# Performance work log

Hardware: AMD Instinct MI355X
Metric: run time of the kernel (lower is better)

Reference implementation:

```python
import jax, jax.numpy as jnp
import numpy as np

B, L, D, H = 2, 2048, 1024, 16
HD = D // H

def setup_inputs() -> dict:
    key = jax.random.key(0)
    ks = jax.random.split(key, 9)
    s = 1.0 / np.sqrt(D)
    return {
        "query": jax.random.normal(ks[0], (B, L, D), dtype=jnp.float32),
        "Wq": jax.random.uniform(ks[1], (D, D), jnp.float32, -s, s),
        "bq": jax.random.uniform(ks[2], (D,), jnp.float32, -s, s),
        "Wk": jax.random.uniform(ks[3], (D, D), jnp.float32, -s, s),
        "bk": jax.random.uniform(ks[4], (D,), jnp.float32, -s, s),
        "Wv": jax.random.uniform(ks[5], (D, D), jnp.float32, -s, s),
        "bv": jax.random.uniform(ks[6], (D,), jnp.float32, -s, s),
        "Wo": jax.random.uniform(ks[7], (D, D), jnp.float32, -s, s),
        "bo": jax.random.uniform(ks[8], (D,), jnp.float32, -s, s),
    }

def reference(query, Wq, bq, Wk, bk, Wv, bv, Wo, bo):
    # self-attention: key_value = query. Linear: x @ W.T + b (torch convention)
    scale = HD ** -0.5
    q = (query @ Wq.T + bq).reshape(B, L, H, HD).transpose(0, 2, 1, 3)  # (B,H,L,hd)
    k = (query @ Wk.T + bk).reshape(B, L, H, HD).transpose(0, 2, 1, 3)
    v = (query @ Wv.T + bv).reshape(B, L, H, HD).transpose(0, 2, 1, 3)
    logits = jnp.einsum('bhqd,bhkd->bhqk', q, k) * scale  # (B,H,Lq,Lk)
    attn = jax.nn.softmax(logits, axis=-1)
    out = jnp.einsum('bhqk,bhkd->bhqd', attn, v)
    out = out.transpose(0, 2, 1, 3).reshape(B, L, D)
    return out @ Wo.T + bo
```

## Files before the change

kernel.cpp:

```cpp
#include <hip/hip_runtime.h>

#define Bc 2
#define Lc 2048
#define Dc 1024
#define Hc 16
#define HDc 64
#define LOG2E 1.44269504088896340736f

typedef __bf16 bf16x8 __attribute__((ext_vector_type(8)));
typedef __bf16 bf16x2 __attribute__((ext_vector_type(2)));
typedef float f32x4 __attribute__((ext_vector_type(4)));
typedef unsigned short u16;
typedef unsigned int u32;
typedef unsigned long long u64;

__device__ __forceinline__ u16 f2bf(float x) {
    union { float f; u32 u; } c; c.f = x;
    u32 u = c.u + 0x7fffu + ((c.u >> 16) & 1u);
    return (u16)(u >> 16);
}

__device__ __forceinline__ u32 pkbf(float a, float b) {
#if __has_builtin(__builtin_amdgcn_cvt_pk_bf16_f32)
    union { bf16x2 v; u32 u; } c;
    c.v = __builtin_amdgcn_cvt_pk_bf16_f32(a, b);
    return c.u;
#else
    return (u32)f2bf(a) | ((u32)f2bf(b) << 16);
#endif
}

__device__ __forceinline__ void g2l16(const void* g, void* l) {
    __builtin_amdgcn_global_load_lds(
        (const __attribute__((address_space(1))) void*)g,
        (__attribute__((address_space(3))) void*)l, 16, 0, 0);
}

__global__ __launch_bounds__(256) void cast_bf16(
    const float* __restrict__ x,
    const float* __restrict__ wq, const float* __restrict__ wk,
    const float* __restrict__ wv, const float* __restrict__ wo,
    u16* __restrict__ xb, u16* __restrict__ wqb, u16* __restrict__ wkb,
    u16* __restrict__ wvb, u16* __restrict__ wob)
{
    const int i = blockIdx.x * 256 + threadIdx.x;
    const float* s; u16* d; int off;
    if (i < 1048576) { s = x; d = xb; off = i; }
    else {
        const int j = i - 1048576;
        const int sel = j >> 18;
        off = j & 262143;
        s = sel == 0 ? wq : sel == 1 ? wk : sel == 2 ? wv : wo;
        d = sel == 0 ? wqb : sel == 1 ? wkb : sel == 2 ? wvb : wob;
    }
    const float4 f = ((const float4*)s)[off];
    ushort4 o;
    o.x = f2bf(f.x); o.y = f2bf(f.y); o.z = f2bf(f.z); o.w = f2bf(f.w);
    ((ushort4*)d)[off] = o;
}

__device__ __forceinline__ void gemm128_body(
    const u16* __restrict__ A, const u16* __restrict__ Bm,
    int row0, int col0, int K,
    f32x4 (&acc)[4][4], u16* As, u16* Bs)
{
    const int tid  = threadIdx.x;
    const int w    = tid >> 6;
    const int lane = tid & 63;
    const int l15  = lane & 15, quad = lane >> 4;
    const int srow = lane >> 3;
    const int sxor = ((lane & 7) ^ srow) << 3;
    const int wm   = (w & 1) << 6, wn = (w >> 1) << 6;
    const int l7   = l15 & 7;

    for (int k0 = 0; k0 < K; k0 += 64) {
        __syncthreads();
#pragma unroll
        for (int s = 0; s < 4; ++s) {
            const int rb = w * 32 + s * 8;
            g2l16(&A [(size_t)(row0 + rb + srow) * K + k0 + sxor], &As[rb * 64]);
            g2l16(&Bm[(size_t)(col0 + rb + srow) * K + k0 + sxor], &Bs[rb * 64]);
        }
        __syncthreads();

#pragma unroll
        for (int kk = 0; kk < 2; ++kk) {
            bf16x8 af[4], bf[4];
#pragma unroll
            for (int i = 0; i < 4; ++i)
                af[i] = *(const bf16x8*)&As[(wm + i * 16 + l15) * 64 +
                                            (((kk * 4 + quad) ^ l7) << 3)];
#pragma unroll
            for (int j = 0; j < 4; ++j)
                bf[j] = *(const bf16x8*)&Bs[(wn + j * 16 + l15) * 64 +
                                            (((kk * 4 + quad) ^ l7) << 3)];
#pragma unroll
            for (int i = 0; i < 4; ++i)
#pragma unroll
                for (int j = 0; j < 4; ++j)
                    acc[i][j] = __builtin_amdgcn_mfma_f32_16x16x32_bf16(
                        af[i], bf[j], acc[i][j], 0, 0, 0);
        }
    }
}

__global__ __launch_bounds__(256) void gemm_qkv_bf16(
    const u16* __restrict__ Xb,
    const u16* __restrict__ Wqb, const u16* __restrict__ Wkb, const u16* __restrict__ Wvb,
    const float* __restrict__ bq, const float* __restrict__ bk, const float* __restrict__ bv,
    u16* __restrict__ qo, u16* __restrict__ ko, u16* __restrict__ vto)
{
    __shared__ __attribute__((aligned(16))) u16 As[128 * 64];
    __shared__ __attribute__((aligned(16))) u16 Bs[128 * 64];

    const int z = blockIdx.z;
    const int tid = threadIdx.x;
    const int w = tid >> 6, lane = tid & 63;
    const int l15 = lane & 15, quad = lane >> 4;
    const int wm = (w & 1) << 6, wn = (w >> 1) << 6;

    f32x4 acc[4][4];
#pragma unroll
    for (int i = 0; i < 4; ++i)
#pragma unroll
        for (int j = 0; j < 4; ++j)
#pragma unroll
            for (int r = 0; r < 4; ++r) acc[i][j][r] = 0.0f;

    if (z == 2) {
        const int row0 = blockIdx.x << 7;
        const int col0 = blockIdx.y << 7;
        gemm128_body(Xb, Wvb, row0, col0, Dc, acc, As, Bs);

        const int b = row0 >> 11;
#pragma unroll
        for (int j = 0; j < 4; ++j) {
            const int n = col0 + wn + j * 16 + l15;
            const float bj = bv[n];
            const int hh = n >> 6, hd = n & 63;
            u16* vbase = vto + (((size_t)(b * Hc + hh) * HDc + hd) << 11);
#pragma unroll
            for (int i = 0; i < 4; ++i) {
                const int l = (row0 + wm + i * 16 + quad * 4) & (Lc - 1);
                uint2 pr;
                pr.x = pkbf(acc[i][j][0] + bj, acc[i][j][1] + bj);
                pr.y = pkbf(acc[i][j][2] + bj, acc[i][j][3] + bj);
                *(uint2*)&vbase[l] = pr;
            }
        }
        return;
    }

    const u16*   W    = z == 0 ? Wqb : Wkb;
    const float* bias = z == 0 ? bq  : bk;
    u16*         outp = z == 0 ? qo  : ko;
    const int row0 = blockIdx.y << 7;
    const int col0 = blockIdx.x << 7;
    gemm128_body(W, Xb, row0, col0, Dc, acc, As, Bs);

    const float qs = z == 0 ? 0.125f * LOG2E : 1.0f;
    const int h = (row0 + wm) >> 6;
    float4 b4[4];
#pragma unroll
    for (int i = 0; i < 4; ++i)
        b4[i] = *(const float4*)&bias[row0 + wm + i * 16 + quad * 4];

#pragma unroll
    for (int j = 0; j < 4; ++j) {
        const int tok = col0 + wn + j * 16 + l15;
        const int bb = tok >> 11, ll = tok & (Lc - 1);
        u16* obase = outp + (((size_t)(bb * Hc + h) * Lc + ll) << 6);
#pragma unroll
        for (int i = 0; i < 4; ++i) {
            uint2 pr;
            pr.x = pkbf((acc[i][j][0] + b4[i].x) * qs, (acc[i][j][1] + b4[i].y) * qs);
            pr.y = pkbf((acc[i][j][2] + b4[i].z) * qs, (acc[i][j][3] + b4[i].w) * qs);
            *(uint2*)&obase[wm ? 0 : 0, i * 16 + quad * 4] = pr;
        }
    }
}

__global__ __launch_bounds__(256) void attn_mfma(
    const u16* __restrict__ q, const u16* __restrict__ k,
    const u16* __restrict__ vt, u16* __restrict__ out)
{
    __shared__ __attribute__((aligned(16))) u16 Ks[2][64 * 32];
    __shared__ __attribute__((aligned(16))) u16 Vs[2][64 * 32];

    const int tid = threadIdx.x;
    const int w = tid >> 6, lane = tid & 63;
    const int l15 = lane & 15, quad = lane >> 4;
    const int bh = blockIdx.x & 31;
    const int qt = blockIdx.x >> 5;
    const int h  = bh & (Hc - 1);
    const int b  = bh >> 4;
    const int l0 = qt << 7;

    const size_t bhs = (size_t)(b * Hc + h) * (Lc * HDc);
    const u16* qb = q  + bhs;
    const u16* kb = k  + bhs;
    const u16* vb = vt + bhs;

    bf16x8 qf[2][2];
#pragma unroll
    for (int mt = 0; mt < 2; ++mt) {
        const size_t row = (size_t)(l0 + w * 32 + mt * 16 + l15) * HDc;
        qf[mt][0] = *(const bf16x8*)&qb[row + quad * 8];
        qf[mt][1] = *(const bf16x8*)&qb[row + 32 + quad * 8];
    }

    const int srow  = lane >> 2;
    const int sunit = lane & 3;
    const int gd = (l15 >> 1) & 3;

    f32x4 oacc[2][4];
    float l_i[2] = {0.0f, 0.0f};
#pragma unroll
    for (int mt = 0; mt < 2; ++mt)
#pragma unroll
        for (int dt = 0; dt < 4; ++dt)
#pragma unroll
            for (int r = 0; r < 4; ++r) oacc[mt][dt][r] = 0.0f;

    for (int kt = 0; kt < Lc; kt += 64) {
        __syncthreads();
#pragma unroll
        for (int i = 0; i < 4; ++i) {
            const int c = w * 4 + i;
            const int p = (c >> 2) & 1, g = c & 3;
            const int row = g * 16 + srow;
            if (c < 8)
                g2l16(&kb[(size_t)(kt + row) * HDc + p * 32 +
                          ((sunit ^ ((row >> 1) & 3)) << 3)],
                      &Ks[p][g * 512]);
            else
                g2l16(&vb[(size_t)row * Lc + kt + p * 32 +
                          ((sunit ^ ((row >> 1) & 3)) << 3)],
                      &Vs[p][g * 512]);
        }
        __syncthreads();

        f32x4 st[2][4];
#pragma unroll
        for (int t = 0; t < 4; ++t) {
            const int j   = t * 16 + l15;
            const int off = j * 32 + ((quad ^ gd) << 3);
            const bf16x8 kf0 = *(const bf16x8*)&Ks[0][off];
            const bf16x8 kf1 = *(const bf16x8*)&Ks[1][off];
#pragma unroll
            for (int mt = 0; mt < 2; ++mt) {
                f32x4 z = {0.0f, 0.0f, 0.0f, 0.0f};
                z = __builtin_amdgcn_mfma_f32_16x16x32_bf16(kf0, qf[mt][0], z, 0, 0, 0);
                st[mt][t] = __builtin_amdgcn_mfma_f32_16x16x32_bf16(kf1, qf[mt][1], z, 0, 0, 0);
            }
        }

        u32 pk[2][4][2];
#pragma unroll
        for (int mt = 0; mt < 2; ++mt) {
            f32x4 s4 = {0.0f, 0.0f, 0.0f, 0.0f};
#pragma unroll
            for (int t = 0; t < 4; ++t) {
                f32x4 p;
#pragma unroll
                for (int r = 0; r < 4; ++r) p[r] = exp2f(st[mt][t][r]);
                s4 += p;
                pk[mt][t][0] = pkbf(p[0], p[1]);
                pk[mt][t][1] = pkbf(p[2], p[3]);
            }
            l_i[mt] += s4[0] + s4[1] + s4[2] + s4[3];
        }

#pragma unroll
        for (int cp = 0; cp < 2; ++cp) {
            union { bf16x8 v; u32 uw[4]; } pf0, pf1;
            pf0.uw[0] = pk[0][2 * cp][0];     pf0.uw[1] = pk[0][2 * cp][1];
            pf0.uw[2] = pk[0][2 * cp + 1][0]; pf0.uw[3] = pk[0][2 * cp + 1][1];
            pf1.uw[0] = pk[1][2 * cp][0];     pf1.uw[1] = pk[1][2 * cp][1];
            pf1.uw[2] = pk[1][2 * cp + 1][0]; pf1.uw[3] = pk[1][2 * cp + 1][1];
#pragma unroll
            for (int dt = 0; dt < 4; ++dt) {
                const int base = (dt * 16 + l15) * 32 + ((quad & 1) << 2);
                union { bf16x8 v; u64 d[2]; } vf;
                vf.d[0] = *(const u64*)&Vs[cp][base + (((quad >> 1) ^ gd) << 3)];
                vf.d[1] = *(const u64*)&Vs[cp][base + (((2 + (quad >> 1)) ^ gd) << 3)];
                oacc[0][dt] = __builtin_amdgcn_mfma_f32_16x16x32_bf16(
                    vf.v, pf0.v, oacc[0][dt], 0, 0, 0);
                oacc[1][dt] = __builtin_amdgcn_mfma_f32_16x16x32_bf16(
                    vf.v, pf1.v, oacc[1][dt], 0, 0, 0);
            }
        }
    }

#pragma unroll
    for (int mt = 0; mt < 2; ++mt) {
        float l = l_i[mt];
        l += __shfl_xor(l, 16);
        l += __shfl_xor(l, 32);
        const float inv = 1.0f / l;
        const int lrow = l0 + w * 32 + mt * 16 + l15;
        u16* ob = out + ((size_t)(b * Lc + lrow)) * Dc + h * HDc;
#pragma unroll
        for (int dt = 0; dt < 4; ++dt) {
            uint2 pr;
            pr.x = pkbf(oacc[mt][dt][0] * inv, oacc[mt][dt][1] * inv);
            pr.y = pkbf(oacc[mt][dt][2] * inv, oacc[mt][dt][3] * inv);
            *(uint2*)&ob[dt * 16 + quad * 4] = pr;
        }
    }
}

__global__ __launch_bounds__(256) void gemm_o_bf16(
    const u16* __restrict__ Ab, const u16* __restrict__ Wob,
    const float* __restrict__ bo, float* __restrict__ out)
{
    __shared__ __attribute__((aligned(16))) u16 As[128 * 64];
    __shared__ __attribute__((aligned(16))) u16 Bs[128 * 64];
    const int row0 = blockIdx.y << 7;
    const int col0 = blockIdx.x << 7;

    f32x4 acc[4][4];
#pragma unroll
    for (int i = 0; i < 4; ++i)
#pragma unroll
        for (int j = 0; j < 4; ++j)
#pragma unroll
            for (int r = 0; r < 4; ++r) acc[i][j][r] = 0.0f;

    gemm128_body(Wob, Ab, row0, col0, Dc, acc, As, Bs);

    const int tid = threadIdx.x;
    const int w = tid >> 6, lane = tid & 63;
    const int l15 = lane & 15, quad = lane >> 4;
    const int wm = (w & 1) << 6, wn = (w >> 1) << 6;

    float4 b4[4];
#pragma unroll
    for (int i = 0; i < 4; ++i)
        b4[i] = *(const float4*)&bo[row0 + wm + i * 16 + quad * 4];

#pragma unroll
    for (int j = 0; j < 4; ++j) {
        const int tok = col0 + wn + j * 16 + l15;
        float* obase = out + (size_t)tok * Dc + row0 + wm;
#pragma unroll
        for (int i = 0; i < 4; ++i) {
            float4 o;
            o.x = acc[i][j][0] + b4[i].x; o.y = acc[i][j][1] + b4[i].y;
            o.z = acc[i][j][2] + b4[i].z; o.w = acc[i][j][3] + b4[i].w;
            *(float4*)&obase[i * 16 + quad * 4] = o;
        }
    }
}

extern "C" void kernel_launch(void* const* d_in, const int* in_sizes, int n_in,
                              void* d_out, int out_size, void* d_ws, size_t ws_size,
                              hipStream_t stream)
{
    const float* query = (const float*)d_in[0];
    const float* Wq = (const float*)d_in[1];
    const float* bq = (const float*)d_in[2];
    const float* Wk = (const float*)d_in[3];
    const float* bk = (const float*)d_in[4];
    const float* Wv = (const float*)d_in[5];
    const float* bv = (const float*)d_in[6];
    const float* Wo = (const float*)d_in[7];
    const float* bo = (const float*)d_in[8];

    u16* ws = (u16*)d_ws;
    const size_t nX = (size_t)Bc * Lc * Dc;
    const size_t nW = (size_t)Dc * Dc;
    u16* xb  = ws;
    u16* wqb = xb + nX;
    u16* wkb = wqb + nW;
    u16* wvb = wkb + nW;
    u16* wob = wvb + nW;
    u16* q_w = wob + nW;
    u16* k_w = q_w + nX;
    u16* vt_w = k_w + nX;
    u16* a_w = vt_w + nX;

    cast_bf16<<<dim3(8192), 256, 0, stream>>>(query, Wq, Wk, Wv, Wo,
                                              xb, wqb, wkb, wvb, wob);
    gemm_qkv_bf16<<<dim3(32, 8, 3), 256, 0, stream>>>(xb, wqb, wkb, wvb,
                                                      bq, bk, bv, q_w, k_w, vt_w);
    attn_mfma<<<dim3(512), 256, 0, stream>>>(q_w, k_w, vt_w, a_w);
    gemm_o_bf16<<<dim3(32, 8), 256, 0, stream>>>(a_w, wob, bo, (float*)d_out);
}
```

Before: 226.4 us.

## Load K and V fragments directly from global memory, dropping LDS staging

The attention kernel no longer stages K and V tiles through shared memory with two block-wide barriers per iteration. Each wave now loads its MFMA operand fragments straight from global memory into registers. This removes the LDS traffic and the syncs, but each of the four waves redundantly fetches the same K/V tiles and relies on L1/L2 to absorb it. The loads are also less coalesced. A cosmetic comma-operator index in the projection store is cleaned up as well.

```diff
diff --git a/kernel.cpp b/kernel.cpp
--- a/kernel.cpp
+++ b/kernel.cpp
@@ -175,7 +175,7 @@
             uint2 pr;
             pr.x = pkbf((acc[i][j][0] + b4[i].x) * qs, (acc[i][j][1] + b4[i].y) * qs);
             pr.y = pkbf((acc[i][j][2] + b4[i].z) * qs, (acc[i][j][3] + b4[i].w) * qs);
-            *(uint2*)&obase[wm ? 0 : 0, i * 16 + quad * 4] = pr;
+            *(uint2*)&obase[i * 16 + quad * 4] = pr;
         }
     }
 }
@@ -184,9 +184,6 @@
     const u16* __restrict__ q, const u16* __restrict__ k,
     const u16* __restrict__ vt, u16* __restrict__ out)
 {
-    __shared__ __attribute__((aligned(16))) u16 Ks[2][64 * 32];
-    __shared__ __attribute__((aligned(16))) u16 Vs[2][64 * 32];
-
     const int tid = threadIdx.x;
     const int w = tid >> 6, lane = tid & 63;
     const int l15 = lane & 15, quad = lane >> 4;
@@ -209,9 +206,8 @@
         qf[mt][1] = *(const bf16x8*)&qb[row + 32 + quad * 8];
     }
 
-    const int srow  = lane >> 2;
-    const int sunit = lane & 3;
-    const int gd = (l15 >> 1) & 3;
+    const u16* kbase = kb + (size_t)l15 * HDc + quad * 8;
+    const u16* vbase = vb + (size_t)l15 * Lc + quad * 4;
 
     f32x4 oacc[2][4];
     float l_i[2] = {0.0f, 0.0f};
@@ -223,37 +219,33 @@
             for (int r = 0; r < 4; ++r) oacc[mt][dt][r] = 0.0f;
 
     for (int kt = 0; kt < Lc; kt += 64) {
-        __syncthreads();
-#pragma unroll
-        for (int i = 0; i < 4; ++i) {
-            const int c = w * 4 + i;
-            const int p = (c >> 2) & 1, g = c & 3;
-            const int row = g * 16 + srow;
-            if (c < 8)
-                g2l16(&kb[(size_t)(kt + row) * HDc + p * 32 +
-                          ((sunit ^ ((row >> 1) & 3)) << 3)],
-                      &Ks[p][g * 512]);
-            else
-                g2l16(&vb[(size_t)row * Lc + kt + p * 32 +
-                          ((sunit ^ ((row >> 1) & 3)) << 3)],
-                      &Vs[p][g * 512]);
-        }
-        __syncthreads();
+        bf16x8 kf[2][4];
+#pragma unroll
+        for (int t = 0; t < 4; ++t) {
+            const u16* kr = kbase + (size_t)(kt + t * 16) * HDc;
+            kf[0][t] = *(const bf16x8*)kr;
+            kf[1][t] = *(const bf16x8*)(kr + 32);
+        }
+        union { bf16x8 v; u64 d[2]; } vf[2][4];
+#pragma unroll
+        for (int dt = 0; dt < 4; ++dt) {
+            const u16* vr = vbase + (size_t)(dt * 16) * Lc + kt;
+#pragma unroll
+            for (int cp = 0; cp < 2; ++cp) {
+                vf[cp][dt].d[0] = *(const u64*)(vr + cp * 32);
+                vf[cp][dt].d[1] = *(const u64*)(vr + cp * 32 + 16);
+            }
+        }
 
         f32x4 st[2][4];
 #pragma unroll
-        for (int t = 0; t < 4; ++t) {
-            const int j   = t * 16 + l15;
-            const int off = j * 32 + ((quad ^ gd) << 3);
-            const bf16x8 kf0 = *(const bf16x8*)&Ks[0][off];
-            const bf16x8 kf1 = *(const bf16x8*)&Ks[1][off];
+        for (int t = 0; t < 4; ++t)
 #pragma unroll
             for (int mt = 0; mt < 2; ++mt) {
                 f32x4 z = {0.0f, 0.0f, 0.0f, 0.0f};
-                z = __builtin_amdgcn_mfma_f32_16x16x32_bf16(kf0, qf[mt][0], z, 0, 0, 0);
-                st[mt][t] = __builtin_amdgcn_mfma_f32_16x16x32_bf16(kf1, qf[mt][1], z, 0, 0, 0);
-            }
-        }
+                z = __builtin_amdgcn_mfma_f32_16x16x32_bf16(kf[0][t], qf[mt][0], z, 0, 0, 0);
+                st[mt][t] = __builtin_amdgcn_mfma_f32_16x16x32_bf16(kf[1][t], qf[mt][1], z, 0, 0, 0);
+            }
 
         u32 pk[2][4][2];
 #pragma unroll
@@ -280,14 +272,10 @@
             pf1.uw[2] = pk[1][2 * cp + 1][0]; pf1.uw[3] = pk[1][2 * cp + 1][1];
 #pragma unroll
             for (int dt = 0; dt < 4; ++dt) {
-                const int base = (dt * 16 + l15) * 32 + ((quad & 1) << 2);
-                union { bf16x8 v; u64 d[2]; } vf;
-                vf.d[0] = *(const u64*)&Vs[cp][base + (((quad >> 1) ^ gd) << 3)];
-                vf.d[1] = *(const u64*)&Vs[cp][base + (((2 + (quad >> 1)) ^ gd) << 3)];
                 oacc[0][dt] = __builtin_amdgcn_mfma_f32_16x16x32_bf16(
-                    vf.v, pf0.v, oacc[0][dt], 0, 0, 0);
+                    vf[cp][dt].v, pf0.v, oacc[0][dt], 0, 0, 0);
                 oacc[1][dt] = __builtin_amdgcn_mfma_f32_16x16x32_bf16(
-                    vf.v, pf1.v, oacc[1][dt], 0, 0, 0);
+                    vf[cp][dt].v, pf1.v, oacc[1][dt], 0, 0, 0);
             }
         }
     }
```

After: 328.3 us. 45.0% more time.
